# Performance work log

Hardware: AMD Instinct MI355X
Metric: run time of the kernel (lower is better)

The kernel has to match this reference:

```python
import jax, jax.numpy as jnp
from jax import lax
import numpy as np

TWO_PI = 2.0 * np.pi

# ---- batched real-amplitude statevector simulator (RY/CNOT only -> real state) ----

def _init_state(batch, n):
    s = jnp.zeros((batch, 2 ** n), dtype=jnp.float32).at[:, 0].set(1.0)
    return s.reshape((batch,) + (2,) * n)

def _ry(state, wire, theta, n):
    # state: (B, 2,...,2); theta: scalar or (B,)
    ax = wire + 1
    h = theta * 0.5
    c = jnp.reshape(jnp.cos(h), (-1,) + (1,) * (n - 1))
    s = jnp.reshape(jnp.sin(h), (-1,) + (1,) * (n - 1))
    s0 = lax.index_in_dim(state, 0, ax, keepdims=False)
    s1 = lax.index_in_dim(state, 1, ax, keepdims=False)
    return jnp.stack([c * s0 - s * s1, s * s0 + c * s1], axis=ax)

def _cnot(state, ctrl, tgt):
    axc, axt = ctrl + 1, tgt + 1
    s0 = lax.index_in_dim(state, 0, axc, keepdims=True)
    s1 = lax.index_in_dim(state, 1, axc, keepdims=True)
    return jnp.concatenate([s0, jnp.flip(s1, axis=axt)], axis=axc)

def _expz(state, wire, n):
    sgn = jnp.reshape(jnp.array([1.0, -1.0], state.dtype),
                      (1,) * (wire + 1) + (2,) + (1,) * (n - wire - 1))
    return jnp.sum(state * state * sgn, axis=tuple(range(1, n + 1)))

# gate lists: ('ry', theta_index, wire) or ('cx', control, target)
EDGE_OPS = [('ry',0,0),('ry',1,1),('cx',0,1),('ry',2,2),('ry',3,3),('cx',3,2),
            ('ry',4,4),('ry',5,5),('cx',4,5),('ry',6,6),('ry',7,7),('cx',7,6),
            ('ry',8,1),('ry',9,2),('cx',1,2),('ry',10,5),('ry',11,6),('cx',6,5),
            ('ry',12,2),('ry',13,5),('cx',2,5),('ry',14,5)]

NODE_OPS = [('ry',0,0),('ry',1,1),('cx',0,1),('ry',2,2),('ry',3,3),('cx',3,2),
            ('ry',4,4),('ry',5,5),('cx',4,5),('ry',6,6),('ry',7,7),('cx',7,6),
            ('ry',8,8),('ry',9,9),('cx',8,9),('ry',10,10),('ry',11,11),('cx',11,10),
            ('ry',12,1),('ry',13,2),('cx',1,2),('ry',14,5),('ry',15,6),('cx',6,5),
            ('ry',16,9),('ry',17,10),('cx',10,9),('ry',18,2),('ry',19,5),('cx',2,5),
            ('ry',20,5),('ry',21,9),('cx',5,9),('ry',22,4)]

def _circuit(angles, theta, ops, n, meas_wire):
    st = _init_state(angles.shape[0], n)
    for i in range(n):  # input encoding RYs, per-sample angles
        st = _ry(st, i, angles[:, i], n)
    for op in ops:
        if op[0] == 'ry':
            st = _ry(st, op[2], theta[op[1]], n)
        else:
            st = _cnot(st, op[1], op[2])
    return _expz(st, meas_wire, n)

# ---- GNN pieces ----

def _edge_net(H, Ri, Ro, theta):
    bo = Ro.T @ H                      # [E,4]
    bi = Ri.T @ H                      # [E,4]
    B = jnp.concatenate([bo, bi], axis=1)  # [E,8]
    return (1.0 - _circuit(B, theta, EDGE_OPS, 8, 5)) * 0.5

def _node_net(H, e, Ri, Ro, theta):
    bo = Ro.T @ H                      # [E,4]
    bi = Ri.T @ H                      # [E,4]
    mi = (Ri * e[None, :]) @ bo        # [N,4]
    mo = (Ro * e[None, :]) @ bi        # [N,4]
    M = jnp.concatenate([mi, mo, H], axis=1)  # [N,12]
    return jnp.pi * (1.0 - _circuit(M, theta, NODE_OPS, 12, 9))

def _gnn(X, Ri, Ro, W_in, b_in, theta_edge, theta_node, n_iters=2):
    H = jnp.concatenate([jax.nn.sigmoid(X @ W_in + b_in) * TWO_PI, X], axis=1)  # [N,4]
    e = _edge_net(H, Ri, Ro, theta_edge)
    for _ in range(n_iters):
        h = _node_net(H, e, Ri, Ro, theta_node)   # [N]
        H = jnp.concatenate([h[:, None], X], axis=1)
        e = _edge_net(H, Ri, Ro, theta_edge)
    return e


def setup_inputs() -> dict:
    key = jax.random.key(0)
    ks = jax.random.split(key, 6)
    N, E = 2048, 4096
    X = jax.random.normal(ks[0], (N, 3), jnp.float32)
    recv = jax.random.randint(ks[1], (E,), 0, N)
    send = jax.random.randint(ks[2], (E,), 0, N)
    cols = jnp.arange(E)
    Ri = jnp.zeros((N, E), jnp.float32).at[recv, cols].set(1.0)
    Ro = jnp.zeros((N, E), jnp.float32).at[send, cols].set(1.0)
    W_in = jax.random.normal(ks[3], (3, 1), jnp.float32)
    b_in = jnp.zeros((1,), jnp.float32)
    theta_edge = jax.random.uniform(ks[4], (15,), jnp.float32, 0.0, TWO_PI)
    theta_node = jax.random.uniform(ks[5], (23,), jnp.float32, 0.0, TWO_PI)
    return {'X': X, 'Ri': Ri, 'Ro': Ro, 'W_in': W_in, 'b_in': b_in,
            'theta_edge': theta_edge, 'theta_node': theta_node}


def reference(X, Ri, Ro, W_in, b_in, theta_edge, theta_node):
    return _gnn(X, Ri, Ro, W_in, b_in, theta_edge, theta_node, n_iters=2)
```

## Files before the change

kernel.cpp:

```cpp
#include <hip/hip_runtime.h>
#include <math.h>

#define N_NODES 2048
#define N_EDGES 4096
#define PI_F 3.14159265358979323846f
#define TWO_PI_F 6.28318530717958647692f

template<int M>
__device__ __forceinline__ float shflx(float v) {
    if constexpr (M == 1) {
        return __int_as_float(__builtin_amdgcn_mov_dpp(
            __float_as_int(v), 0xB1, 0xF, 0xF, false));
    } else if constexpr (M == 2) {
        return __int_as_float(__builtin_amdgcn_mov_dpp(
            __float_as_int(v), 0x4E, 0xF, 0xF, false));
    } else if constexpr (M == 8) {
        return __int_as_float(__builtin_amdgcn_mov_dpp(
            __float_as_int(v), 0x128, 0xF, 0xF, false));
    } else {
        return __shfl_xor(v, M, 64);
    }
}

__device__ __forceinline__ float wave_sum(float p) {
    p += shflx<32>(p); p += shflx<16>(p); p += shflx<8>(p);
    p += shflx<4>(p);  p += shflx<2>(p);  p += shflx<1>(p);
    return p;
}


template<int NA, int B>
__device__ __forceinline__ void ry_j(float* a, float c, float s) {
#pragma unroll
    for (int j = 0; j < NA; ++j) {
        if ((j & (1 << B)) == 0) {
            int k = j | (1 << B);
            float x0 = a[j], x1 = a[k];
            a[j] = c * x0 - s * x1;
            a[k] = s * x0 + c * x1;
        }
    }
}

template<int NA, int MASK>
__device__ __forceinline__ void ry_l(float* a, float c, float s, int lane) {
    float ss = (lane & MASK) ? s : -s;
#pragma unroll
    for (int j = 0; j < NA; ++j) {
        float p = shflx<MASK>(a[j]);
        a[j] = c * a[j] + ss * p;
    }
}

template<int NA, int BC, int BT>
__device__ __forceinline__ void cx_jj(float* a) {
#pragma unroll
    for (int j = 0; j < NA; ++j) {
        if ((j & (1 << BC)) && !(j & (1 << BT))) {
            int k = j | (1 << BT);
            float t = a[j]; a[j] = a[k]; a[k] = t;
        }
    }
}

template<int NA, int MC, int BT>
__device__ __forceinline__ void cx_lj(float* a, int lane) {
    bool sel = (lane & MC) != 0;
#pragma unroll
    for (int j = 0; j < NA; ++j) {
        if ((j & (1 << BT)) == 0) {
            int k = j | (1 << BT);
            float t0 = a[j], t1 = a[k];
            a[j] = sel ? t1 : t0;
            a[k] = sel ? t0 : t1;
        }
    }
}

template<int NA, int MC, int MT>
__device__ __forceinline__ void cx_ll(float* a, int lane) {
    bool sel = (lane & MC) != 0;
#pragma unroll
    for (int j = 0; j < NA; ++j) {
        float p = shflx<MT>(a[j]);
        a[j] = sel ? p : a[j];
    }
}

__global__ __launch_bounds__(256) void k_setup(
        const float* __restrict__ X, const float* __restrict__ Ri,
        const float* __restrict__ Ro, const float* __restrict__ W,
        const float* __restrict__ b, const float* __restrict__ te,
        const float* __restrict__ tn,
        int* __restrict__ send, int* __restrict__ recv, float* __restrict__ H,
        float* __restrict__ htrig,
        float* __restrict__ maccA, float* __restrict__ maccB,
        float* __restrict__ trig) {
    int tid = blockIdx.x * blockDim.x + threadIdx.x;
    if (tid < N_NODES) {
        float x0 = X[tid*3+0], x1 = X[tid*3+1], x2 = X[tid*3+2];
        float z = x0*W[0] + x1*W[1] + x2*W[2] + b[0];
        float sg = 1.0f / (1.0f + __expf(-z));
        float h = sg * TWO_PI_F;
        H[tid*4+0] = h;
        H[tid*4+1] = x0; H[tid*4+2] = x1; H[tid*4+3] = x2;
        float c0,s0,c1,s1,c2,s2,c3,s3;
        __sincosf(0.5f*h,  &s0, &c0);
        __sincosf(0.5f*x0, &s1, &c1);
        __sincosf(0.5f*x1, &s2, &c2);
        __sincosf(0.5f*x2, &s3, &c3);
        ((float4*)htrig)[tid*2+0] = make_float4(c0, s0, c1, s1);
        ((float4*)htrig)[tid*2+1] = make_float4(c2, s2, c3, s3);
    }
    if (tid < N_NODES * 8) { maccA[tid] = 0.f; maccB[tid] = 0.f; }
    if (tid >= 4096 && tid < 4096 + 15) {
        int i = tid - 4096; float s, c;
        __sincosf(0.5f * te[i], &s, &c);
        trig[i] = c; trig[16 + i] = s;
    }
    if (tid >= 4224 && tid < 4224 + 23) {
        int i = tid - 4224; float s, c;
        __sincosf(0.5f * tn[i], &s, &c);
        trig[32 + i] = c; trig[56 + i] = s;
    }
    const float4 vi = ((const float4*)Ri)[tid];
    const float4 vo = ((const float4*)Ro)[tid];
    int base = tid * 4;
    int n = base >> 12;
    int e = base & (N_EDGES - 1);
    if (vi.x != 0.f) recv[e+0] = n;
    if (vi.y != 0.f) recv[e+1] = n;
    if (vi.z != 0.f) recv[e+2] = n;
    if (vi.w != 0.f) recv[e+3] = n;
    if (vo.x != 0.f) send[e+0] = n;
    if (vo.y != 0.f) send[e+1] = n;
    if (vo.z != 0.f) send[e+2] = n;
    if (vo.w != 0.f) send[e+3] = n;
}

template<bool SCATTER>
__global__ __launch_bounds__(256) void k_edge(
        const float* __restrict__ H, const float* __restrict__ htrig,
        const int* __restrict__ send, const int* __restrict__ recv,
        const float* __restrict__ trig,
        float* __restrict__ out, float* __restrict__ macc) {
    int e = (blockIdx.x * blockDim.x + threadIdx.x) >> 6;
    int lane = threadIdx.x & 63;
    int si = send[e], ri = recv[e];
    float4 t0 = ((const float4*)htrig)[si*2+0];
    float4 t1 = ((const float4*)htrig)[si*2+1];
    float4 t2 = ((const float4*)htrig)[ri*2+0];
    float4 t3 = ((const float4*)htrig)[ri*2+1];
    float ec[8] = {t0.x, t0.z, t1.x, t1.z, t2.x, t2.z, t3.x, t3.z};
    float es[8] = {t0.y, t0.w, t1.y, t1.w, t2.y, t2.w, t3.y, t3.w};

    float lp;
    {
        float f0 = (lane&32) ? es[0] : ec[0];
        float f1 = (lane&16) ? es[1] : ec[1];
        float f3 = (lane& 8) ? es[3] : ec[3];
        float f4 = (lane& 4) ? es[4] : ec[4];
        float f6 = (lane& 2) ? es[6] : ec[6];
        float f7 = (lane& 1) ? es[7] : ec[7];
        lp = f0*f1*f3*f4*f6*f7;
    }
    float a[4];
    a[0] = lp;
    a[1] = a[0]*es[5]; a[0] *= ec[5];
    a[2] = a[0]*es[2]; a[3] = a[1]*es[2];
    a[0] *= ec[2];     a[1] *= ec[2];

    const float* tc = trig;
    const float* ts = trig + 16;

    ry_l<4,32>(a, tc[0], ts[0], lane);
    ry_l<4,16>(a, tc[1], ts[1], lane);
    cx_ll<4,32,16>(a, lane);
    ry_j<4,1>(a, tc[2], ts[2]);
    ry_l<4,8>(a, tc[3], ts[3], lane);
    cx_lj<4,8,1>(a, lane);
    ry_l<4,4>(a, tc[4], ts[4], lane);
    ry_j<4,0>(a, tc[5], ts[5]);
    cx_lj<4,4,0>(a, lane);
    ry_l<4,2>(a, tc[6], ts[6], lane);
    ry_l<4,1>(a, tc[7], ts[7], lane);
    cx_ll<4,1,2>(a, lane);
    ry_l<4,16>(a, tc[8], ts[8], lane);
    ry_j<4,1>(a, tc[9], ts[9]);
    cx_lj<4,16,1>(a, lane);
    ry_j<4,0>(a, tc[10], ts[10]);
    ry_l<4,2>(a, tc[11], ts[11], lane);
    cx_lj<4,2,0>(a, lane);
    ry_j<4,1>(a, tc[12], ts[12]);
    ry_j<4,0>(a, tc[13], ts[13]);
    cx_jj<4,1,0>(a);
    ry_j<4,0>(a, tc[14], ts[14]);

    float p = (a[0]*a[0] + a[2]*a[2]) - (a[1]*a[1] + a[3]*a[3]);
    p = wave_sum(p);
    float ev = (1.0f - p) * 0.5f;

    if (SCATTER) {
        if (lane < 8) {
            float4 hs = ((const float4*)H)[si];
            float4 hr = ((const float4*)H)[ri];
            float B[8] = {hs.x, hs.y, hs.z, hs.w, hr.x, hr.y, hr.z, hr.w};
            float bv = B[0];
            if (lane == 1) bv = B[1]; if (lane == 2) bv = B[2]; if (lane == 3) bv = B[3];
            if (lane == 4) bv = B[4]; if (lane == 5) bv = B[5]; if (lane == 6) bv = B[6];
            if (lane == 7) bv = B[7];
            int idx = (lane < 4) ? (ri*8 + lane) : (si*8 + 4 + (lane & 3));
            atomicAdd(&macc[idx], ev * bv);
        }
    } else {
        if (lane == 0) out[e] = ev;
    }
}

__global__ __launch_bounds__(256) void k_node(
        const float* __restrict__ macc, float* __restrict__ H,
        float* __restrict__ htrig, const float* __restrict__ trig) {
    __shared__ float part[2][2];
    int wb   = threadIdx.x >> 6;
    int lane = threadIdx.x & 63;
    int pair = wb >> 1;
    int par  = wb & 1;
    int n = blockIdx.x * 2 + pair;

    float4 m0 = ((const float4*)macc)[n*2];
    float4 m1 = ((const float4*)macc)[n*2+1];
    float M[8] = {m0.x, m0.y, m0.z, m0.w, m1.x, m1.y, m1.z, m1.w};

    float mc[12], ms[12];
#pragma unroll
    for (int k = 0; k < 8; ++k) __sincosf(0.5f * M[k], &ms[k], &mc[k]);
    {
        float4 t0 = ((const float4*)htrig)[n*2+0];
        float4 t1 = ((const float4*)htrig)[n*2+1];
        mc[8] = t0.x; ms[8] = t0.y; mc[9]  = t0.z; ms[9]  = t0.w;
        mc[10]= t1.x; ms[10]= t1.y; mc[11] = t1.z; ms[11] = t1.w;
    }

    float lp;
    {
        float f0 = (lane&32) ? ms[0] : mc[0];
        float f1 = (lane&16) ? ms[1] : mc[1];
        float f3 = (lane& 8) ? ms[3] : mc[3];
        float f4 = (lane& 4) ? ms[4] : mc[4];
        float f7 = (lane& 2) ? ms[7] : mc[7];
        float f8 = (lane& 1) ? ms[8] : mc[8];
        lp = f0*f1*f3*f4*f7*f8;
    }
    float a[32];
    a[0] = lp;
    {
        const int jw[5] = {10, 9, 6, 5, 2};
#pragma unroll
        for (int bnum = 0; bnum < 5; ++bnum) {
            int sz = 1 << bnum;
            float cw = mc[jw[bnum]], sw = ms[jw[bnum]];
#pragma unroll
            for (int k = 0; k < 32; ++k) {
                if (k < sz) {
                    a[k + sz] = a[k] * sw;
                    a[k] *= cw;
                }
            }
        }
    }

    const float* tc = trig + 32;
    const float* ts = trig + 56;

    ry_l<32,32>(a, tc[0], ts[0], lane);
    ry_l<32,16>(a, tc[1], ts[1], lane);
    cx_ll<32,32,16>(a, lane);
    ry_j<32,4>(a, tc[2], ts[2]);
    ry_l<32,8>(a, tc[3], ts[3], lane);
    cx_lj<32,8,4>(a, lane);
    ry_l<32,4>(a, tc[4], ts[4], lane);
    ry_j<32,3>(a, tc[5], ts[5]);
    cx_lj<32,4,3>(a, lane);
    ry_j<32,2>(a, tc[6], ts[6]);
    ry_l<32,2>(a, tc[7], ts[7], lane);
    cx_lj<32,2,2>(a, lane);
    ry_l<32,1>(a, tc[8], ts[8], lane);
    ry_j<32,1>(a, tc[9], ts[9]);
    cx_lj<32,1,1>(a, lane);
    ry_j<32,0>(a, tc[10], ts[10]);
    {
        float f = par ? (ts[11]*mc[11] + tc[11]*ms[11])
                      : (tc[11]*mc[11] - ts[11]*ms[11]);
#pragma unroll
        for (int j = 0; j < 32; ++j) a[j] *= f;
    }
    if (par) {
#pragma unroll
        for (int j = 0; j < 32; j += 2) {
            float t = a[j]; a[j] = a[j+1]; a[j+1] = t;
        }
    }
    ry_l<32,16>(a, tc[12], ts[12], lane);
    ry_j<32,4>(a, tc[13], ts[13]);
    cx_lj<32,16,4>(a, lane);
    ry_j<32,3>(a, tc[14], ts[14]);
    ry_j<32,2>(a, tc[15], ts[15]);
    cx_jj<32,2,3>(a);
    ry_j<32,1>(a, tc[16], ts[16]);
    ry_j<32,0>(a, tc[17], ts[17]);
    cx_jj<32,0,1>(a);
    ry_j<32,4>(a, tc[18], ts[18]);
    ry_j<32,3>(a, tc[19], ts[19]);
    cx_jj<32,4,3>(a);
    ry_j<32,3>(a, tc[20], ts[20]);
    ry_j<32,1>(a, tc[21], ts[21]);
    cx_jj<32,3,1>(a);

    float p = 0.f;
#pragma unroll
    for (int j = 0; j < 32; ++j) {
        float q = a[j]*a[j];
        p += (j & 2) ? -q : q;
    }
    p = wave_sum(p);
    if (lane == 0) part[pair][par] = p;
    __syncthreads();
    if (lane == 0 && par == 0) {
        float h = PI_F * (1.0f - (part[pair][0] + part[pair][1]));
        H[n*4+0] = h;
        float sh, ch;
        __sincosf(0.5f * h, &sh, &ch);
        htrig[n*8+0] = ch;
        htrig[n*8+1] = sh;
    }
}

extern "C" void kernel_launch(void* const* d_in, const int* in_sizes, int n_in,
                              void* d_out, int out_size, void* d_ws, size_t ws_size,
                              hipStream_t stream) {
    const float* X  = (const float*)d_in[0];
    const float* Ri = (const float*)d_in[1];
    const float* Ro = (const float*)d_in[2];
    const float* W  = (const float*)d_in[3];
    const float* b  = (const float*)d_in[4];
    const float* te = (const float*)d_in[5];
    const float* tn = (const float*)d_in[6];
    float* out = (float*)d_out;

    int*   send  = (int*)d_ws;
    int*   recv  = send + N_EDGES;
    float* H     = (float*)(recv + N_EDGES);
    float* htrig = H + N_NODES * 4;
    float* ebuf  = htrig + N_NODES * 8;
    float* maccA = ebuf + N_EDGES;
    float* maccB = maccA + N_NODES * 8;
    float* trig  = maccB + N_NODES * 8;

    int total4 = (N_NODES * N_EDGES) / 4;
    k_setup<<<total4 / 256, 256, 0, stream>>>(X, Ri, Ro, W, b, te, tn,
                                              send, recv, H, htrig,
                                              maccA, maccB, trig);
    k_edge<true ><<<N_EDGES / 4, 256, 0, stream>>>(H, htrig, send, recv, trig, ebuf, maccA);
    k_node<<<N_NODES / 2, 256, 0, stream>>>(maccA, H, htrig, trig);
    k_edge<true ><<<N_EDGES / 4, 256, 0, stream>>>(H, htrig, send, recv, trig, ebuf, maccB);
    k_node<<<N_NODES / 2, 256, 0, stream>>>(maccB, H, htrig, trig);
    k_edge<false><<<N_EDGES / 4, 256, 0, stream>>>(H, htrig, send, recv, trig, out, nullptr);
}
```

Measured before the change: 147.1 us.

## Factorize circuits into per-node subproducts and fuse iterations into one persistent megakernel

The edge circuit is split algebraically into independent 4-qubit subcircuits whose Z/X expectations are computed once per node and published. Each edge's expectation then becomes a cheap product of these per-node values, and the node circuit is factored the same way. The five edge/node launches are replaced by one 96-block persistent kernel. Inside it, edge and node blocks synchronise through per-node arrival counters and epoch flags with spin-waits, and the accumulators are zeroed with a memset. This removes most launch overhead and the wave-wide statevector simulation, but it depends on all 96 blocks being co-resident and on atomic ordering for correctness.

```diff
diff --git a/kernel.cpp b/kernel.cpp
--- a/kernel.cpp
+++ b/kernel.cpp
@@ -6,84 +6,92 @@
 #define PI_F 3.14159265358979323846f
 #define TWO_PI_F 6.28318530717958647692f
 
+__device__ __forceinline__ float agent_load(const float* p) {
+    return __hip_atomic_load(p, __ATOMIC_RELAXED, __HIP_MEMORY_SCOPE_AGENT);
+}
+__device__ __forceinline__ void agent_store(float* p, float v) {
+    __hip_atomic_store(p, v, __ATOMIC_RELAXED, __HIP_MEMORY_SCOPE_AGENT);
+}
+__device__ __forceinline__ void agent_store_i(int* p, int v) {
+    __hip_atomic_store(p, v, __ATOMIC_RELAXED, __HIP_MEMORY_SCOPE_AGENT);
+}
+__device__ __forceinline__ void spin_ge(const int* p, int v) {
+    while (__hip_atomic_load(p, __ATOMIC_RELAXED, __HIP_MEMORY_SCOPE_AGENT) < v)
+        __builtin_amdgcn_s_sleep(2);
+    asm volatile("" ::: "memory");
+}
+
+
 template<int M>
-__device__ __forceinline__ float shflx(float v) {
-    if constexpr (M == 1) {
-        return __int_as_float(__builtin_amdgcn_mov_dpp(
-            __float_as_int(v), 0xB1, 0xF, 0xF, false));
-    } else if constexpr (M == 2) {
-        return __int_as_float(__builtin_amdgcn_mov_dpp(
-            __float_as_int(v), 0x4E, 0xF, 0xF, false));
-    } else if constexpr (M == 8) {
-        return __int_as_float(__builtin_amdgcn_mov_dpp(
-            __float_as_int(v), 0x128, 0xF, 0xF, false));
-    } else {
-        return __shfl_xor(v, M, 64);
-    }
-}
-
-__device__ __forceinline__ float wave_sum(float p) {
-    p += shflx<32>(p); p += shflx<16>(p); p += shflx<8>(p);
-    p += shflx<4>(p);  p += shflx<2>(p);  p += shflx<1>(p);
-    return p;
-}
-
-
-template<int NA, int B>
-__device__ __forceinline__ void ry_j(float* a, float c, float s) {
-#pragma unroll
-    for (int j = 0; j < NA; ++j) {
-        if ((j & (1 << B)) == 0) {
-            int k = j | (1 << B);
-            float x0 = a[j], x1 = a[k];
-            a[j] = c * x0 - s * x1;
-            a[k] = s * x0 + c * x1;
+__device__ __forceinline__ void ry16(float* a, float c, float s) {
+#pragma unroll
+    for (int i = 0; i < 16; ++i)
+        if (!(i & M)) {
+            int j = i | M;
+            float x0 = a[i], x1 = a[j];
+            a[i] = c * x0 - s * x1;
+            a[j] = s * x0 + c * x1;
         }
-    }
-}
-
-template<int NA, int MASK>
-__device__ __forceinline__ void ry_l(float* a, float c, float s, int lane) {
-    float ss = (lane & MASK) ? s : -s;
-#pragma unroll
-    for (int j = 0; j < NA; ++j) {
-        float p = shflx<MASK>(a[j]);
-        a[j] = c * a[j] + ss * p;
-    }
-}
-
-template<int NA, int BC, int BT>
-__device__ __forceinline__ void cx_jj(float* a) {
-#pragma unroll
-    for (int j = 0; j < NA; ++j) {
-        if ((j & (1 << BC)) && !(j & (1 << BT))) {
-            int k = j | (1 << BT);
-            float t = a[j]; a[j] = a[k]; a[k] = t;
+}
+template<int MC, int MT>
+__device__ __forceinline__ void cx16(float* a) {
+#pragma unroll
+    for (int i = 0; i < 16; ++i)
+        if ((i & MC) && !(i & MT)) {
+            int j = i | MT;
+            float t = a[i]; a[i] = a[j]; a[j] = t;
         }
-    }
-}
-
-template<int NA, int MC, int BT>
-__device__ __forceinline__ void cx_lj(float* a, int lane) {
-    bool sel = (lane & MC) != 0;
-#pragma unroll
-    for (int j = 0; j < NA; ++j) {
-        if ((j & (1 << BT)) == 0) {
-            int k = j | (1 << BT);
-            float t0 = a[j], t1 = a[k];
-            a[j] = sel ? t1 : t0;
-            a[k] = sel ? t0 : t1;
-        }
-    }
-}
-
-template<int NA, int MC, int MT>
-__device__ __forceinline__ void cx_ll(float* a, int lane) {
-    bool sel = (lane & MC) != 0;
-#pragma unroll
-    for (int j = 0; j < NA; ++j) {
-        float p = shflx<MT>(a[j]);
-        a[j] = sel ? p : a[j];
+}
+
+template<bool BTYPE>
+__device__ __forceinline__ void sub16(const float* ic, const float* is,
+                                      const float* thc, const float* ths,
+                                      float& z, float& x) {
+    float a[16];
+    a[0] = ic[3]; a[1] = is[3];
+#pragma unroll
+    for (int i = 0; i < 2; ++i) { a[i | 2] = a[i] * is[2]; a[i] *= ic[2]; }
+#pragma unroll
+    for (int i = 0; i < 4; ++i) { a[i | 4] = a[i] * is[1]; a[i] *= ic[1]; }
+#pragma unroll
+    for (int i = 0; i < 8; ++i) { a[i | 8] = a[i] * is[0]; a[i] *= ic[0]; }
+    ry16<8>(a, thc[0], ths[0]);
+    ry16<4>(a, thc[1], ths[1]);
+    cx16<8, 4>(a);
+    ry16<2>(a, thc[2], ths[2]);
+    ry16<1>(a, thc[3], ths[3]);
+    cx16<1, 2>(a);
+    ry16<4>(a, thc[4], ths[4]);
+    ry16<2>(a, thc[5], ths[5]);
+    if (BTYPE) { cx16<2, 4>(a); ry16<4>(a, thc[6], ths[6]); }
+    else       { cx16<4, 2>(a); ry16<2>(a, thc[6], ths[6]); }
+    const int m = BTYPE ? 4 : 2;
+    z = 0.f; x = 0.f;
+#pragma unroll
+    for (int i = 0; i < 16; ++i) z += (i & m) ? -a[i] * a[i] : a[i] * a[i];
+    if (BTYPE) {
+#pragma unroll
+        for (int i = 0; i < 16; ++i) if (!(i & 4)) x += a[i] * a[i | 4];
+        x *= 2.f;
+    }
+}
+
+__device__ __forceinline__ void edge_pub(
+        float chh, float shh, const float* cxv, const float* sxv,
+        const float* teC, const float* teS,
+        float& zA, float& zB, float& xB) {
+    float ic[4] = {chh, cxv[0], cxv[1], cxv[2]};
+    float is[4] = {shh, sxv[0], sxv[1], sxv[2]};
+    float dmy;
+    {
+        float thc[7] = {teC[0], teC[1], teC[2], teC[3], teC[8], teC[9], teC[12]};
+        float ths[7] = {teS[0], teS[1], teS[2], teS[3], teS[8], teS[9], teS[12]};
+        sub16<false>(ic, is, thc, ths, zA, dmy);
+    }
+    {
+        float thc[7] = {teC[4], teC[5], teC[6], teC[7], teC[10], teC[11], teC[13]};
+        float ths[7] = {teS[4], teS[5], teS[6], teS[7], teS[10], teS[11], teS[13]};
+        sub16<true>(ic, is, thc, ths, zB, xB);
     }
 }
 
@@ -93,26 +101,27 @@
         const float* __restrict__ b, const float* __restrict__ te,
         const float* __restrict__ tn,
         int* __restrict__ send, int* __restrict__ recv, float* __restrict__ H,
-        float* __restrict__ htrig,
-        float* __restrict__ maccA, float* __restrict__ maccB,
-        float* __restrict__ trig) {
+        float* __restrict__ pub, float* __restrict__ trig,
+        int* __restrict__ deg) {
     int tid = blockIdx.x * blockDim.x + threadIdx.x;
     if (tid < N_NODES) {
         float x0 = X[tid*3+0], x1 = X[tid*3+1], x2 = X[tid*3+2];
         float z = x0*W[0] + x1*W[1] + x2*W[2] + b[0];
         float sg = 1.0f / (1.0f + __expf(-z));
         float h = sg * TWO_PI_F;
-        H[tid*4+0] = h;
-        H[tid*4+1] = x0; H[tid*4+2] = x1; H[tid*4+3] = x2;
-        float c0,s0,c1,s1,c2,s2,c3,s3;
-        __sincosf(0.5f*h,  &s0, &c0);
-        __sincosf(0.5f*x0, &s1, &c1);
-        __sincosf(0.5f*x1, &s2, &c2);
-        __sincosf(0.5f*x2, &s3, &c3);
-        ((float4*)htrig)[tid*2+0] = make_float4(c0, s0, c1, s1);
-        ((float4*)htrig)[tid*2+1] = make_float4(c2, s2, c3, s3);
-    }
-    if (tid < N_NODES * 8) { maccA[tid] = 0.f; maccB[tid] = 0.f; }
+        ((float4*)H)[tid] = make_float4(h, x0, x1, x2);
+        float chh, shh, cxv[3], sxv[3];
+        __sincosf(0.5f*h,  &shh, &chh);
+        __sincosf(0.5f*x0, &sxv[0], &cxv[0]);
+        __sincosf(0.5f*x1, &sxv[1], &cxv[1]);
+        __sincosf(0.5f*x2, &sxv[2], &cxv[2]);
+        float teC[14], teS[14];
+#pragma unroll
+        for (int k = 0; k < 14; ++k) __sincosf(0.5f*te[k], &teS[k], &teC[k]);
+        float zA, zB, xB;
+        edge_pub(chh, shh, cxv, sxv, teC, teS, zA, zB, xB);
+        pub[tid*4+0] = zA; pub[tid*4+1] = zB; pub[tid*4+2] = xB;
+    }
     if (tid >= 4096 && tid < 4096 + 15) {
         int i = tid - 4096; float s, c;
         __sincosf(0.5f * te[i], &s, &c);
@@ -128,210 +137,120 @@
     int base = tid * 4;
     int n = base >> 12;
     int e = base & (N_EDGES - 1);
-    if (vi.x != 0.f) recv[e+0] = n;
-    if (vi.y != 0.f) recv[e+1] = n;
-    if (vi.z != 0.f) recv[e+2] = n;
-    if (vi.w != 0.f) recv[e+3] = n;
-    if (vo.x != 0.f) send[e+0] = n;
-    if (vo.y != 0.f) send[e+1] = n;
-    if (vo.z != 0.f) send[e+2] = n;
-    if (vo.w != 0.f) send[e+3] = n;
-}
-
-template<bool SCATTER>
-__global__ __launch_bounds__(256) void k_edge(
-        const float* __restrict__ H, const float* __restrict__ htrig,
+    int cnt = 0;
+    if (vi.x != 0.f) { recv[e+0] = n; ++cnt; }
+    if (vi.y != 0.f) { recv[e+1] = n; ++cnt; }
+    if (vi.z != 0.f) { recv[e+2] = n; ++cnt; }
+    if (vi.w != 0.f) { recv[e+3] = n; ++cnt; }
+    if (vo.x != 0.f) { send[e+0] = n; ++cnt; }
+    if (vo.y != 0.f) { send[e+1] = n; ++cnt; }
+    if (vo.z != 0.f) { send[e+2] = n; ++cnt; }
+    if (vo.w != 0.f) { send[e+3] = n; ++cnt; }
+    if (cnt) atomicAdd(&deg[n], cnt);
+}
+
+__device__ __forceinline__ void scatter8(float ev, const float4& Hs, const float4& Hr,
+                                         int si, int ri,
+                                         float* __restrict__ macc, int* __restrict__ arr) {
+    atomicAdd(&macc[ri*8+0], ev*Hs.x); atomicAdd(&macc[ri*8+1], ev*Hs.y);
+    atomicAdd(&macc[ri*8+2], ev*Hs.z); atomicAdd(&macc[ri*8+3], ev*Hs.w);
+    atomicAdd(&macc[si*8+4], ev*Hr.x); atomicAdd(&macc[si*8+5], ev*Hr.y);
+    atomicAdd(&macc[si*8+6], ev*Hr.z); atomicAdd(&macc[si*8+7], ev*Hr.w);
+    asm volatile("s_waitcnt vmcnt(0)" ::: "memory");
+    atomicAdd(&arr[ri], 1); atomicAdd(&arr[si], 1);
+}
+
+__global__ __launch_bounds__(64) void k_mega(
+        float* __restrict__ H, float* __restrict__ pub,
         const int* __restrict__ send, const int* __restrict__ recv,
         const float* __restrict__ trig,
-        float* __restrict__ out, float* __restrict__ macc) {
-    int e = (blockIdx.x * blockDim.x + threadIdx.x) >> 6;
-    int lane = threadIdx.x & 63;
-    int si = send[e], ri = recv[e];
-    float4 t0 = ((const float4*)htrig)[si*2+0];
-    float4 t1 = ((const float4*)htrig)[si*2+1];
-    float4 t2 = ((const float4*)htrig)[ri*2+0];
-    float4 t3 = ((const float4*)htrig)[ri*2+1];
-    float ec[8] = {t0.x, t0.z, t1.x, t1.z, t2.x, t2.z, t3.x, t3.z};
-    float es[8] = {t0.y, t0.w, t1.y, t1.w, t2.y, t2.w, t3.y, t3.w};
-
-    float lp;
-    {
-        float f0 = (lane&32) ? es[0] : ec[0];
-        float f1 = (lane&16) ? es[1] : ec[1];
-        float f3 = (lane& 8) ? es[3] : ec[3];
-        float f4 = (lane& 4) ? es[4] : ec[4];
-        float f6 = (lane& 2) ? es[6] : ec[6];
-        float f7 = (lane& 1) ? es[7] : ec[7];
-        lp = f0*f1*f3*f4*f6*f7;
-    }
-    float a[4];
-    a[0] = lp;
-    a[1] = a[0]*es[5]; a[0] *= ec[5];
-    a[2] = a[0]*es[2]; a[3] = a[1]*es[2];
-    a[0] *= ec[2];     a[1] *= ec[2];
-
-    const float* tc = trig;
-    const float* ts = trig + 16;
-
-    ry_l<4,32>(a, tc[0], ts[0], lane);
-    ry_l<4,16>(a, tc[1], ts[1], lane);
-    cx_ll<4,32,16>(a, lane);
-    ry_j<4,1>(a, tc[2], ts[2]);
-    ry_l<4,8>(a, tc[3], ts[3], lane);
-    cx_lj<4,8,1>(a, lane);
-    ry_l<4,4>(a, tc[4], ts[4], lane);
-    ry_j<4,0>(a, tc[5], ts[5]);
-    cx_lj<4,4,0>(a, lane);
-    ry_l<4,2>(a, tc[6], ts[6], lane);
-    ry_l<4,1>(a, tc[7], ts[7], lane);
-    cx_ll<4,1,2>(a, lane);
-    ry_l<4,16>(a, tc[8], ts[8], lane);
-    ry_j<4,1>(a, tc[9], ts[9]);
-    cx_lj<4,16,1>(a, lane);
-    ry_j<4,0>(a, tc[10], ts[10]);
-    ry_l<4,2>(a, tc[11], ts[11], lane);
-    cx_lj<4,2,0>(a, lane);
-    ry_j<4,1>(a, tc[12], ts[12]);
-    ry_j<4,0>(a, tc[13], ts[13]);
-    cx_jj<4,1,0>(a);
-    ry_j<4,0>(a, tc[14], ts[14]);
-
-    float p = (a[0]*a[0] + a[2]*a[2]) - (a[1]*a[1] + a[3]*a[3]);
-    p = wave_sum(p);
-    float ev = (1.0f - p) * 0.5f;
-
-    if (SCATTER) {
-        if (lane < 8) {
-            float4 hs = ((const float4*)H)[si];
-            float4 hr = ((const float4*)H)[ri];
-            float B[8] = {hs.x, hs.y, hs.z, hs.w, hr.x, hr.y, hr.z, hr.w};
-            float bv = B[0];
-            if (lane == 1) bv = B[1]; if (lane == 2) bv = B[2]; if (lane == 3) bv = B[3];
-            if (lane == 4) bv = B[4]; if (lane == 5) bv = B[5]; if (lane == 6) bv = B[6];
-            if (lane == 7) bv = B[7];
-            int idx = (lane < 4) ? (ri*8 + lane) : (si*8 + 4 + (lane & 3));
-            atomicAdd(&macc[idx], ev * bv);
+        float* __restrict__ maccA, float* __restrict__ maccB,
+        int* __restrict__ arrA, int* __restrict__ arrB,
+        int* __restrict__ epoch, const int* __restrict__ deg,
+        float* __restrict__ out) {
+    int lane = threadIdx.x;
+    int blk  = blockIdx.x;
+
+    if (blk < 64) {
+        int e = blk * 64 + lane;
+        int si = send[e], ri = recv[e];
+        float4 Hs = ((const float4*)H)[si];
+        float4 Hr = ((const float4*)H)[ri];
+        float c14 = trig[14], s14 = trig[30];
+        float C14 = c14*c14 - s14*s14;
+        float S14 = 2.f*c14*s14;
+
+        float zA = pub[si*4+0], zB = pub[ri*4+1], xB = pub[ri*4+2];
+        float ev = 0.5f*(1.f - (C14*zA*zB - S14*xB));
+        scatter8(ev, Hs, Hr, si, ri, maccA, arrA);
+
+        spin_ge(epoch + si, 1); spin_ge(epoch + ri, 1);
+        zA = agent_load(&pub[si*4+0]);
+        zB = agent_load(&pub[ri*4+1]);
+        xB = agent_load(&pub[ri*4+2]);
+        Hs.x = agent_load(&H[si*4]);
+        Hr.x = agent_load(&H[ri*4]);
+        ev = 0.5f*(1.f - (C14*zA*zB - S14*xB));
+        scatter8(ev, Hs, Hr, si, ri, maccB, arrB);
+
+        spin_ge(epoch + si, 2); spin_ge(epoch + ri, 2);
+        zA = agent_load(&pub[si*4+0]);
+        zB = agent_load(&pub[ri*4+1]);
+        xB = agent_load(&pub[ri*4+2]);
+        out[e] = 0.5f*(1.f - (C14*zA*zB - S14*xB));
+    } else {
+        int n = (blk - 64) * 64 + lane;
+        float4 Hn = ((const float4*)H)[n];
+        float chh, shh, cxv[3], sxv[3];
+        __sincosf(0.5f*Hn.x, &shh, &chh);
+        __sincosf(0.5f*Hn.y, &sxv[0], &cxv[0]);
+        __sincosf(0.5f*Hn.z, &sxv[1], &cxv[1]);
+        __sincosf(0.5f*Hn.w, &sxv[2], &cxv[2]);
+        int dg = deg[n];
+        const float* teC = trig;      const float* teS = trig + 16;
+        const float* tnC = trig + 32; const float* tnS = trig + 56;
+        float C20 = tnC[20]*tnC[20] - tnS[20]*tnS[20];
+        float S20 = 2.f*tnC[20]*tnS[20];
+
+        for (int it = 0; it < 2; ++it) {
+            const float* mc_ = it ? maccB : maccA;
+            const int*   ar  = it ? arrB  : arrA;
+            spin_ge(ar + n, dg);
+            float M[8], mC[8], mS[8];
+#pragma unroll
+            for (int k = 0; k < 8; ++k) M[k] = agent_load(mc_ + n*8 + k);
+#pragma unroll
+            for (int k = 0; k < 8; ++k) __sincosf(0.5f*M[k], &mS[k], &mC[k]);
+            float zA1, zA2, xA2, zB9, dmy;
+            {
+                float thc[7] = {tnC[0],tnC[1],tnC[2],tnC[3],tnC[12],tnC[13],tnC[18]};
+                float ths[7] = {tnS[0],tnS[1],tnS[2],tnS[3],tnS[12],tnS[13],tnS[18]};
+                sub16<false>(&mC[0], &mS[0], thc, ths, zA1, dmy);
+            }
+            {
+                float thc[7] = {tnC[4],tnC[5],tnC[6],tnC[7],tnC[14],tnC[15],tnC[19]};
+                float ths[7] = {tnS[4],tnS[5],tnS[6],tnS[7],tnS[14],tnS[15],tnS[19]};
+                sub16<true>(&mC[4], &mS[4], thc, ths, zA2, xA2);
+            }
+            {
+                float ic[4] = {chh, cxv[0], cxv[1], cxv[2]};
+                float is[4] = {shh, sxv[0], sxv[1], sxv[2]};
+                float thc[7] = {tnC[8],tnC[9],tnC[10],tnC[11],tnC[16],tnC[17],tnC[21]};
+                float ths[7] = {tnS[8],tnS[9],tnS[10],tnS[11],tnS[16],tnS[17],tnS[21]};
+                sub16<true>(ic, is, thc, ths, zB9, dmy);
+            }
+            float p9 = (C20*zA1*zA2 - S20*xA2) * zB9;
+            float h = PI_F * (1.f - p9);
+            __sincosf(0.5f*h, &shh, &chh);
+            float zAe, zBe, xBe;
+            edge_pub(chh, shh, cxv, sxv, teC, teS, zAe, zBe, xBe);
+            agent_store(&pub[n*4+0], zAe);
+            agent_store(&pub[n*4+1], zBe);
+            agent_store(&pub[n*4+2], xBe);
+            agent_store(&H[n*4], h);
+            asm volatile("s_waitcnt vmcnt(0)" ::: "memory");
+            agent_store_i(epoch + n, it + 1);
         }
-    } else {
-        if (lane == 0) out[e] = ev;
-    }
-}
-
-__global__ __launch_bounds__(256) void k_node(
-        const float* __restrict__ macc, float* __restrict__ H,
-        float* __restrict__ htrig, const float* __restrict__ trig) {
-    __shared__ float part[2][2];
-    int wb   = threadIdx.x >> 6;
-    int lane = threadIdx.x & 63;
-    int pair = wb >> 1;
-    int par  = wb & 1;
-    int n = blockIdx.x * 2 + pair;
-
-    float4 m0 = ((const float4*)macc)[n*2];
-    float4 m1 = ((const float4*)macc)[n*2+1];
-    float M[8] = {m0.x, m0.y, m0.z, m0.w, m1.x, m1.y, m1.z, m1.w};
-
-    float mc[12], ms[12];
-#pragma unroll
-    for (int k = 0; k < 8; ++k) __sincosf(0.5f * M[k], &ms[k], &mc[k]);
-    {
-        float4 t0 = ((const float4*)htrig)[n*2+0];
-        float4 t1 = ((const float4*)htrig)[n*2+1];
-        mc[8] = t0.x; ms[8] = t0.y; mc[9]  = t0.z; ms[9]  = t0.w;
-        mc[10]= t1.x; ms[10]= t1.y; mc[11] = t1.z; ms[11] = t1.w;
-    }
-
-    float lp;
-    {
-        float f0 = (lane&32) ? ms[0] : mc[0];
-        float f1 = (lane&16) ? ms[1] : mc[1];
-        float f3 = (lane& 8) ? ms[3] : mc[3];
-        float f4 = (lane& 4) ? ms[4] : mc[4];
-        float f7 = (lane& 2) ? ms[7] : mc[7];
-        float f8 = (lane& 1) ? ms[8] : mc[8];
-        lp = f0*f1*f3*f4*f7*f8;
-    }
-    float a[32];
-    a[0] = lp;
-    {
-        const int jw[5] = {10, 9, 6, 5, 2};
-#pragma unroll
-        for (int bnum = 0; bnum < 5; ++bnum) {
-            int sz = 1 << bnum;
-            float cw = mc[jw[bnum]], sw = ms[jw[bnum]];
-#pragma unroll
-            for (int k = 0; k < 32; ++k) {
-                if (k < sz) {
-                    a[k + sz] = a[k] * sw;
-                    a[k] *= cw;
-                }
-            }
-        }
-    }
-
-    const float* tc = trig + 32;
-    const float* ts = trig + 56;
-
-    ry_l<32,32>(a, tc[0], ts[0], lane);
-    ry_l<32,16>(a, tc[1], ts[1], lane);
-    cx_ll<32,32,16>(a, lane);
-    ry_j<32,4>(a, tc[2], ts[2]);
-    ry_l<32,8>(a, tc[3], ts[3], lane);
-    cx_lj<32,8,4>(a, lane);
-    ry_l<32,4>(a, tc[4], ts[4], lane);
-    ry_j<32,3>(a, tc[5], ts[5]);
-    cx_lj<32,4,3>(a, lane);
-    ry_j<32,2>(a, tc[6], ts[6]);
-    ry_l<32,2>(a, tc[7], ts[7], lane);
-    cx_lj<32,2,2>(a, lane);
-    ry_l<32,1>(a, tc[8], ts[8], lane);
-    ry_j<32,1>(a, tc[9], ts[9]);
-    cx_lj<32,1,1>(a, lane);
-    ry_j<32,0>(a, tc[10], ts[10]);
-    {
-        float f = par ? (ts[11]*mc[11] + tc[11]*ms[11])
-                      : (tc[11]*mc[11] - ts[11]*ms[11]);
-#pragma unroll
-        for (int j = 0; j < 32; ++j) a[j] *= f;
-    }
-    if (par) {
-#pragma unroll
-        for (int j = 0; j < 32; j += 2) {
-            float t = a[j]; a[j] = a[j+1]; a[j+1] = t;
-        }
-    }
-    ry_l<32,16>(a, tc[12], ts[12], lane);
-    ry_j<32,4>(a, tc[13], ts[13]);
-    cx_lj<32,16,4>(a, lane);
-    ry_j<32,3>(a, tc[14], ts[14]);
-    ry_j<32,2>(a, tc[15], ts[15]);
-    cx_jj<32,2,3>(a);
-    ry_j<32,1>(a, tc[16], ts[16]);
-    ry_j<32,0>(a, tc[17], ts[17]);
-    cx_jj<32,0,1>(a);
-    ry_j<32,4>(a, tc[18], ts[18]);
-    ry_j<32,3>(a, tc[19], ts[19]);
-    cx_jj<32,4,3>(a);
-    ry_j<32,3>(a, tc[20], ts[20]);
-    ry_j<32,1>(a, tc[21], ts[21]);
-    cx_jj<32,3,1>(a);
-
-    float p = 0.f;
-#pragma unroll
-    for (int j = 0; j < 32; ++j) {
-        float q = a[j]*a[j];
-        p += (j & 2) ? -q : q;
-    }
-    p = wave_sum(p);
-    if (lane == 0) part[pair][par] = p;
-    __syncthreads();
-    if (lane == 0 && par == 0) {
-        float h = PI_F * (1.0f - (part[pair][0] + part[pair][1]));
-        H[n*4+0] = h;
-        float sh, ch;
-        __sincosf(0.5f * h, &sh, &ch);
-        htrig[n*8+0] = ch;
-        htrig[n*8+1] = sh;
     }
 }
 
@@ -350,19 +269,20 @@
     int*   send  = (int*)d_ws;
     int*   recv  = send + N_EDGES;
     float* H     = (float*)(recv + N_EDGES);
-    float* htrig = H + N_NODES * 4;
-    float* ebuf  = htrig + N_NODES * 8;
-    float* maccA = ebuf + N_EDGES;
+    float* pub   = H + N_NODES * 4;
+    float* trig  = pub + N_NODES * 4;
+    float* maccA = trig + 128;
     float* maccB = maccA + N_NODES * 8;
-    float* trig  = maccB + N_NODES * 8;
-
+    int*   arrA  = (int*)(maccB + N_NODES * 8);
+    int*   arrB  = arrA + N_NODES;
+    int*   epoch = arrB + N_NODES;
+    int*   deg   = epoch + N_NODES;
+    size_t zbytes = (size_t)(2 * N_NODES * 8 + 4 * N_NODES) * sizeof(float);
+
+    hipMemsetAsync((void*)maccA, 0, zbytes, stream);
     int total4 = (N_NODES * N_EDGES) / 4;
     k_setup<<<total4 / 256, 256, 0, stream>>>(X, Ri, Ro, W, b, te, tn,
-                                              send, recv, H, htrig,
-                                              maccA, maccB, trig);
-    k_edge<true ><<<N_EDGES / 4, 256, 0, stream>>>(H, htrig, send, recv, trig, ebuf, maccA);
-    k_node<<<N_NODES / 2, 256, 0, stream>>>(maccA, H, htrig, trig);
-    k_edge<true ><<<N_EDGES / 4, 256, 0, stream>>>(H, htrig, send, recv, trig, ebuf, maccB);
-    k_node<<<N_NODES / 2, 256, 0, stream>>>(maccB, H, htrig, trig);
-    k_edge<false><<<N_EDGES / 4, 256, 0, stream>>>(H, htrig, send, recv, trig, out, nullptr);
-}
+                                              send, recv, H, pub, trig, deg);
+    k_mega<<<96, 64, 0, stream>>>(H, pub, send, recv, trig,
+                                  maccA, maccB, arrA, arrB, epoch, deg, out);
+}
```

Result: faster. 123.5 us (-16.1%).
